# Optimization experiments

Hardware: AMD Instinct MI355X
Metric: run time of the kernel (lower is better)

## Reference

```python
import jax, jax.numpy as jnp
import numpy as np

N, E = 40000, 640000
IN, HID, OUT = 128, 128, 128


def _lin(key, fan_in, fan_out):
    bound = 1.0 / np.sqrt(fan_in)
    kw, kb = jax.random.split(key)
    W = jax.random.uniform(kw, (fan_in, fan_out), jnp.float32, -bound, bound)
    b = jax.random.uniform(kb, (fan_out,), jnp.float32, -bound, bound)
    return W, b


def setup_inputs() -> dict:
    key = jax.random.key(0)
    ks = jax.random.split(key, 10)
    node_feat = jax.random.normal(ks[0], (N, IN), jnp.float32)
    coord_feat = jax.random.normal(ks[1], (N, 3), jnp.float32)
    src = jax.random.randint(ks[2], (E,), 0, N, jnp.int32)
    dst = jax.random.randint(ks[3], (E,), 0, N, jnp.int32)
    # edge_mlp: Linear(2*IN+1 -> HID), SiLU, Linear(HID -> HID), SiLU
    We1, be1 = _lin(ks[4], 2 * IN + 1, HID)
    We2, be2 = _lin(ks[5], HID, HID)
    # node_mlp: Linear(IN+HID -> HID), SiLU, Linear(HID -> OUT)
    Wn1, bn1 = _lin(ks[6], IN + HID, HID)
    Wn2, bn2 = _lin(ks[7], HID, OUT)
    # coord_mlp: Linear(HID -> HID), SiLU, Linear(HID -> 1, bias=False)
    Wc1, bc1 = _lin(ks[8], HID, HID)
    Wc2, _ = _lin(ks[9], HID, 1)
    return {"node_feat": node_feat, "coord_feat": coord_feat, "src": src, "dst": dst,
            "We1": We1, "be1": be1, "We2": We2, "be2": be2,
            "Wn1": Wn1, "bn1": bn1, "Wn2": Wn2, "bn2": bn2,
            "Wc1": Wc1, "bc1": bc1, "Wc2": Wc2}


def reference(node_feat, coord_feat, src, dst,
              We1, be1, We2, be2, Wn1, bn1, Wn2, bn2, Wc1, bc1, Wc2):
    n = node_feat.shape[0]
    # edge gather: u_sub_v gives x_src - x_dst
    x_diff = coord_feat[src] - coord_feat[dst]                       # (E, 3)
    dist = jnp.sqrt(jnp.sum(x_diff * x_diff, axis=-1, keepdims=True))  # (E, 1)
    x_dir = x_diff / (dist + 1e-7)
    f = jnp.concatenate([node_feat[src], node_feat[dst], dist], axis=-1)  # (E, 2*IN+1)
    msg_h = jax.nn.silu(jax.nn.silu(f @ We1 + be1) @ We2 + be2)      # (E, HID)
    coef = jax.nn.silu(msg_h @ Wc1 + bc1) @ Wc2                      # (E, 1)
    msg_x = coef * x_dir                                             # (E, 3)
    # scatter-reduce to destination nodes: sum for h, mean for x
    h_neigh = jax.ops.segment_sum(msg_h, dst, num_segments=n)        # (N, HID)
    cnt = jax.ops.segment_sum(jnp.ones((dst.shape[0], 1), msg_x.dtype), dst, num_segments=n)
    x_neigh = jax.ops.segment_sum(msg_x, dst, num_segments=n) / jnp.maximum(cnt, 1.0)
    h = jax.nn.silu(jnp.concatenate([node_feat, h_neigh], axis=-1) @ Wn1 + bn1) @ Wn2 + bn2
    return h, coord_feat + x_neigh
```

## Files before the change

### kernel.cpp

```cpp
#include <hip/hip_runtime.h>
#include <hip/hip_bf16.h>
#include <math.h>
#include <stdint.h>

#define N_NODES 40000
#define N_EDGES 640000

typedef short short8 __attribute__((ext_vector_type(8)));
typedef float f32x4 __attribute__((ext_vector_type(4)));

__device__ __forceinline__ float silu(float x) {
    return __fdividef(x, 1.0f + __expf(-x));
}

__device__ __forceinline__ unsigned short f2bf(float f) {
    unsigned u = __float_as_uint(f);
    u += 0x7FFF + ((u >> 16) & 1);
    return (unsigned short)(u >> 16);
}
__device__ __forceinline__ float bf2f(unsigned short h) {
    return __uint_as_float(((unsigned)h) << 16);
}
__device__ __forceinline__ unsigned pk2bf(float a, float b) {
    __hip_bfloat162 h = __float22bfloat162_rn(make_float2(a, b));
    unsigned u;
    __builtin_memcpy(&u, &h, 4);
    return u;
}

__global__ __launch_bounds__(1024) void k_scan(const int* __restrict__ deg,
                                               int* __restrict__ row_start) {
    __shared__ int wsum[16];
    const int t = threadIdx.x;
    const int lane = t & 63, wid = t >> 6;
    int base = 0;
    if (t == 0) row_start[0] = 0;
    for (int off = 0; off < N_NODES; off += 1024) {
        int x = (off + t < N_NODES) ? deg[off + t] : 0;
#pragma unroll
        for (int s = 1; s < 64; s <<= 1) {
            const int u = __shfl_up(x, s, 64);
            if (lane >= s) x += u;
        }
        if (lane == 63) wsum[wid] = x;
        __syncthreads();
        if (wid == 0) {
            int ws = (lane < 16) ? wsum[lane] : 0;
#pragma unroll
            for (int s = 1; s < 16; s <<= 1) {
                const int u = __shfl_up(ws, s, 64);
                if (lane >= s) ws += u;
            }
            if (lane < 16) wsum[lane] = ws;
        }
        __syncthreads();
        const int wbase = (wid > 0) ? wsum[wid - 1] : 0;
        const int total = wsum[15];
        if (off + t < N_NODES) row_start[off + t + 1] = base + wbase + x;
        base += total;
        __syncthreads();
    }
}

__global__ __launch_bounds__(256) void k_fill(const int* __restrict__ dst,
                                              const int* __restrict__ row_start,
                                              int* __restrict__ cursor,
                                              int* __restrict__ elist) {
    const int e = blockIdx.x * 256 + threadIdx.x;
    if (e < N_EDGES) {
        const int d = dst[e];
        const int p = atomicAdd(&cursor[d], 1);
        elist[row_start[d] + p] = e;
    }
}

__global__ __launch_bounds__(128) void k_pack2(
    const float* __restrict__ We1, const float* __restrict__ We2,
    const float* __restrict__ Wc1, const float* __restrict__ Wn1,
    const float* __restrict__ Wn2,
    unsigned short* __restrict__ Wt_e1, unsigned short* __restrict__ Wt_e2,
    unsigned short* __restrict__ Wt_c1, unsigned short* __restrict__ Wt_n1,
    unsigned short* __restrict__ Wt_n2,
    int* __restrict__ deg, int* __restrict__ cursor, float* __restrict__ xs,
    float* __restrict__ hn) {
    const int b = blockIdx.x;
    const int t = threadIdx.x;
    Wt_e1[b * 128 + t] = f2bf(We1[(size_t)((b >> 7) * 128 + t) * 128 + (b & 127)]);
    if (b < 128) {
        Wt_e2[b * 128 + t] = f2bf(We2[(size_t)t * 128 + b]);
        Wt_c1[b * 128 + t] = f2bf(Wc1[(size_t)t * 128 + b]);
        Wt_n2[b * 128 + t] = f2bf(Wn2[(size_t)t * 128 + b]);
        Wt_n1[b * 256 + t] = f2bf(Wn1[(size_t)t * 128 + b]);
        Wt_n1[b * 256 + 128 + t] = f2bf(Wn1[(size_t)(128 + t) * 128 + b]);
    }
    const int gid = b * 128 + t;
    for (int i = gid; i < N_NODES; i += 32768) { deg[i] = 0; cursor[i] = 0; }
    for (int i = gid; i < N_NODES * 4; i += 32768) xs[i] = 0.0f;
    float4* hz = (float4*)hn;
    const float4 z4 = {0.f, 0.f, 0.f, 0.f};
    for (int i = gid; i < N_NODES * 32; i += 32768) hz[i] = z4;
}

__global__ __launch_bounds__(256) void k_cntpre(
    const float* __restrict__ nf, const unsigned short* __restrict__ Wt_e1,
    unsigned short* __restrict__ Pc,
    const int* __restrict__ dst, int* __restrict__ deg) {
    __shared__ __align__(16) unsigned short sNF[32][136];
    const int t = threadIdx.x;
    const int node0 = blockIdx.x * 32;
    {
        const int e0 = (blockIdx.x * 256 + t) * 2;
        const int d0 = dst[e0], d1 = dst[e0 + 1];
        atomicAdd(&deg[d0], 1);
        atomicAdd(&deg[d1], 1);
    }
    {
        const int m = t >> 3, kc = (t & 7) * 16;
        const float* sp = &nf[(size_t)(node0 + m) * 128 + kc];
        const float4 v0 = *(const float4*)(sp + 0);
        const float4 v1 = *(const float4*)(sp + 4);
        const float4 v2 = *(const float4*)(sp + 8);
        const float4 v3 = *(const float4*)(sp + 12);
        int4 o0, o1;
        o0.x = pk2bf(v0.x, v0.y); o0.y = pk2bf(v0.z, v0.w);
        o0.z = pk2bf(v1.x, v1.y); o0.w = pk2bf(v1.z, v1.w);
        o1.x = pk2bf(v2.x, v2.y); o1.y = pk2bf(v2.z, v2.w);
        o1.z = pk2bf(v3.x, v3.y); o1.w = pk2bf(v3.z, v3.w);
        *(int4*)&sNF[m][kc] = o0;
        *(int4*)&sNF[m][kc + 8] = o1;
    }
    __syncthreads();

    const int w = t >> 6, l = t & 63, c = l & 15, quad = l >> 4;
    const int n0 = w * 64;

    f32x4 acc[2][4];
#pragma unroll
    for (int mt = 0; mt < 2; mt++)
#pragma unroll
        for (int tile = 0; tile < 4; tile++) acc[mt][tile] = (f32x4){0.f, 0.f, 0.f, 0.f};

#pragma unroll
    for (int k0 = 0; k0 < 128; k0 += 32) {
        const short8 a0 = *(const short8*)&sNF[c][k0 + quad * 8];
        const short8 a1 = *(const short8*)&sNF[16 + c][k0 + quad * 8];
#pragma unroll
        for (int tile = 0; tile < 4; tile++) {
            const short8 b = *(const short8*)(Wt_e1 +
                ((size_t)(n0 + tile * 16 + c) << 7) + k0 + quad * 8);
            acc[0][tile] = __builtin_amdgcn_mfma_f32_16x16x32_bf16(a0, b, acc[0][tile], 0, 0, 0);
            acc[1][tile] = __builtin_amdgcn_mfma_f32_16x16x32_bf16(a1, b, acc[1][tile], 0, 0, 0);
        }
    }
#pragma unroll
    for (int mt = 0; mt < 2; mt++)
#pragma unroll
        for (int tile = 0; tile < 4; tile++) {
            const int col = n0 + tile * 16 + c;
            const unsigned p01 = pk2bf(acc[mt][tile][0], acc[mt][tile][1]);
            const unsigned p23 = pk2bf(acc[mt][tile][2], acc[mt][tile][3]);
            const int row = node0 + mt * 16 + quad * 4;
            Pc[(size_t)(row + 0) * 256 + col] = (unsigned short)p01;
            Pc[(size_t)(row + 1) * 256 + col] = (unsigned short)(p01 >> 16);
            Pc[(size_t)(row + 2) * 256 + col] = (unsigned short)p23;
            Pc[(size_t)(row + 3) * 256 + col] = (unsigned short)(p23 >> 16);
        }
}

__global__ __launch_bounds__(512) void k_edge5(
    const unsigned short* __restrict__ Pc, const float* __restrict__ coord,
    const int* __restrict__ src, const int* __restrict__ dst,
    const int* __restrict__ elist,
    const float* __restrict__ We1, const float* __restrict__ be1,
    const unsigned short* __restrict__ Wt_e2, const float* __restrict__ be2,
    const unsigned short* __restrict__ Wt_c1, const float* __restrict__ bc1,
    const float* __restrict__ Wc2,
    float* __restrict__ h_neigh, float* __restrict__ xs) {
    __shared__ __align__(16) unsigned short sT[128][136];
    __shared__ float scoefp[8][32];
    __shared__ float sw[128], sb[128];
    __shared__ float sdist[128];
    __shared__ float sxd[128][3];
    __shared__ int ssrc[128];
    __shared__ int sdst[128];

    const int t = threadIdx.x;
    const int e0 = blockIdx.x * 128;

    if (t < 128) {
        const int eid = elist[e0 + t];
        const int s = src[eid], d = dst[eid];
        ssrc[t] = s; sdst[t] = d;
        const float dx = coord[3 * s + 0] - coord[3 * d + 0];
        const float dy = coord[3 * s + 1] - coord[3 * d + 1];
        const float dz = coord[3 * s + 2] - coord[3 * d + 2];
        const float dist = sqrtf(dx * dx + dy * dy + dz * dz);
        sdist[t] = dist;
        const float inv = __fdividef(1.0f, dist + 1e-7f);
        sxd[t][0] = dx * inv; sxd[t][1] = dy * inv; sxd[t][2] = dz * inv;
    } else if (t < 160) {
        ((float4*)sw)[t - 128] = ((const float4*)(We1 + 256 * 128))[t - 128];
    } else if (t < 192) {
        ((float4*)sb)[t - 160] = ((const float4*)be1)[t - 160];
    }
    __syncthreads();

    {
        const int e = t >> 2;
        const int kc = (t & 3) * 32;
        const int s = ssrc[e], d = sdst[e];
        const float dist = sdist[e];
        const unsigned short* p1 = Pc + (size_t)s * 256 + kc;
        const unsigned short* p2 = Pc + (size_t)d * 256 + 128 + kc;
        short8 a[4], b[4];
#pragma unroll
        for (int i = 0; i < 4; i++) {
            a[i] = *(const short8*)(p1 + i * 8);
            b[i] = *(const short8*)(p2 + i * 8);
        }
#pragma unroll
        for (int i = 0; i < 4; i++) {
            float v[8];
#pragma unroll
            for (int kk = 0; kk < 8; kk++) {
                const int k = kc + i * 8 + kk;
                v[kk] = silu(bf2f((unsigned short)a[i][kk]) + bf2f((unsigned short)b[i][kk])
                             + dist * sw[k] + sb[k]);
            }
            int4 o;
            o.x = pk2bf(v[0], v[1]); o.y = pk2bf(v[2], v[3]);
            o.z = pk2bf(v[4], v[5]); o.w = pk2bf(v[6], v[7]);
            *(int4*)&sT[e][kc + i * 8] = o;
        }
    }
    __syncthreads();

    const int w = t >> 6;
    const int l = t & 63;
    const int h = w & 3;
    const int H = w >> 2;
    const int m0 = h * 32;
    const int n0 = H * 64;
    const int c = l & 15;
    const int quad = l >> 4;

    f32x4 acc1[2][4];
#pragma unroll
    for (int mt = 0; mt < 2; mt++)
#pragma unroll
        for (int tile = 0; tile < 4; tile++) acc1[mt][tile] = (f32x4){0.f, 0.f, 0.f, 0.f};
#pragma unroll
    for (int k0 = 0; k0 < 128; k0 += 32) {
        const short8 a0 = *(const short8*)&sT[m0 + c][k0 + quad * 8];
        const short8 a1 = *(const short8*)&sT[m0 + 16 + c][k0 + quad * 8];
#pragma unroll
        for (int tile = 0; tile < 4; tile++) {
            const short8 b = *(const short8*)(Wt_e2 +
                ((size_t)(n0 + tile * 16 + c) << 7) + k0 + quad * 8);
            acc1[0][tile] = __builtin_amdgcn_mfma_f32_16x16x32_bf16(a0, b, acc1[0][tile], 0, 0, 0);
            acc1[1][tile] = __builtin_amdgcn_mfma_f32_16x16x32_bf16(a1, b, acc1[1][tile], 0, 0, 0);
        }
    }
    __syncthreads();

#pragma unroll
    for (int mt = 0; mt < 2; mt++)
#pragma unroll
        for (int tile = 0; tile < 4; tile++) {
            const int col = n0 + tile * 16 + c;
            const float bb = be2[col];
            const unsigned p01 = pk2bf(silu(acc1[mt][tile][0] + bb), silu(acc1[mt][tile][1] + bb));
            const unsigned p23 = pk2bf(silu(acc1[mt][tile][2] + bb), silu(acc1[mt][tile][3] + bb));
            const int row = m0 + mt * 16 + quad * 4;
            sT[row + 0][col] = (unsigned short)p01;
            sT[row + 1][col] = (unsigned short)(p01 >> 16);
            sT[row + 2][col] = (unsigned short)p23;
            sT[row + 3][col] = (unsigned short)(p23 >> 16);
        }
    __syncthreads();

    {
        const int j = t & 127;
        const int q = t >> 7;
        const int eb = q * 32;
        float acc = bf2f(sT[eb][j]);
        int prev = sdst[eb];
        for (int e2 = eb + 1; e2 < eb + 32; e2++) {
            const int de = sdst[e2];
            if (de != prev) {
                atomicAdd(&h_neigh[(size_t)prev * 128 + j], acc);
                acc = 0.0f;
                prev = de;
            }
            acc += bf2f(sT[e2][j]);
        }
        atomicAdd(&h_neigh[(size_t)prev * 128 + j], acc);
    }

    {
        f32x4 acc[2][4];
#pragma unroll
        for (int mt = 0; mt < 2; mt++)
#pragma unroll
            for (int tile = 0; tile < 4; tile++) acc[mt][tile] = (f32x4){0.f, 0.f, 0.f, 0.f};
#pragma unroll
        for (int k0 = 0; k0 < 128; k0 += 32) {
            const short8 a0 = *(const short8*)&sT[m0 + c][k0 + quad * 8];
            const short8 a1 = *(const short8*)&sT[m0 + 16 + c][k0 + quad * 8];
#pragma unroll
            for (int tile = 0; tile < 4; tile++) {
                const short8 b = *(const short8*)(Wt_c1 +
                    ((size_t)(n0 + tile * 16 + c) << 7) + k0 + quad * 8);
                acc[0][tile] = __builtin_amdgcn_mfma_f32_16x16x32_bf16(a0, b, acc[0][tile], 0, 0, 0);
                acc[1][tile] = __builtin_amdgcn_mfma_f32_16x16x32_bf16(a1, b, acc[1][tile], 0, 0, 0);
            }
        }
        float part[2][4] = {{0.f, 0.f, 0.f, 0.f}, {0.f, 0.f, 0.f, 0.f}};
#pragma unroll
        for (int tile = 0; tile < 4; tile++) {
            const int col = n0 + tile * 16 + c;
            const float bc = bc1[col];
            const float wc = Wc2[col];
#pragma unroll
            for (int mt = 0; mt < 2; mt++)
#pragma unroll
                for (int r = 0; r < 4; r++)
                    part[mt][r] += silu(acc[mt][tile][r] + bc) * wc;
        }
#pragma unroll
        for (int off = 1; off < 16; off <<= 1) {
#pragma unroll
            for (int mt = 0; mt < 2; mt++)
#pragma unroll
                for (int r = 0; r < 4; r++)
                    part[mt][r] += __shfl_xor(part[mt][r], off, 64);
        }
        if (c == 0) {
#pragma unroll
            for (int mt = 0; mt < 2; mt++)
#pragma unroll
                for (int r = 0; r < 4; r++)
                    scoefp[w][mt * 16 + quad * 4 + r] = part[mt][r];
        }
    }

    if (l < 3) {
        const int cc = l;
        const int eb = h * 32;
        float acc = scoefp[w][0] * sxd[eb][cc];
        int prev = sdst[eb];
        for (int e2 = eb + 1; e2 < eb + 32; e2++) {
            const int de = sdst[e2];
            if (de != prev) {
                atomicAdd(&xs[(size_t)prev * 4 + cc], acc);
                acc = 0.0f;
                prev = de;
            }
            acc += scoefp[w][e2 & 31] * sxd[e2][cc];
        }
        atomicAdd(&xs[(size_t)prev * 4 + cc], acc);
    }
}

__global__ __launch_bounds__(256) void k_node(
    const float* __restrict__ nf, const float* __restrict__ coord,
    const float* __restrict__ hn, const float* __restrict__ xs,
    const int* __restrict__ row_start,
    const unsigned short* __restrict__ Wt_n1, const float* __restrict__ bn1,
    const unsigned short* __restrict__ Wt_n2, const float* __restrict__ bn2,
    float* __restrict__ out_h, float* __restrict__ out_x) {
    __shared__ __align__(16) unsigned short sAB[32][264];
    __shared__ __align__(16) unsigned short sH[32][136];
    const int t = threadIdx.x;
    const int node0 = blockIdx.x * 32;
    {
        const int m = t >> 3, kc = (t & 7) * 32;
        const float* base = (kc < 128) ? &nf[(size_t)(node0 + m) * 128 + kc]
                                       : &hn[(size_t)(node0 + m) * 128 + (kc - 128)];
#pragma unroll
        for (int kk = 0; kk < 32; kk += 8) {
            const float4 v0 = *(const float4*)(base + kk);
            const float4 v1 = *(const float4*)(base + kk + 4);
            int4 o;
            o.x = pk2bf(v0.x, v0.y); o.y = pk2bf(v0.z, v0.w);
            o.z = pk2bf(v1.x, v1.y); o.w = pk2bf(v1.z, v1.w);
            *(int4*)&sAB[m][kc + kk] = o;
        }
    }
    if (t < 96) {
        const int m = t / 3, cc = t - m * 3;
        const int i = node0 + m;
        const float cnt = (float)(row_start[i + 1] - row_start[i]);
        out_x[(size_t)i * 3 + cc] =
            coord[(size_t)i * 3 + cc] + __fdividef(xs[(size_t)i * 4 + cc], fmaxf(cnt, 1.0f));
    }
    __syncthreads();

    const int w = t >> 6, l = t & 63, c = l & 15, quad = l >> 4;
    const int n0 = w * 32;

    {
        f32x4 acc[2][2];
#pragma unroll
        for (int mt = 0; mt < 2; mt++)
#pragma unroll
            for (int tile = 0; tile < 2; tile++) acc[mt][tile] = (f32x4){0.f, 0.f, 0.f, 0.f};
#pragma unroll
        for (int k0 = 0; k0 < 256; k0 += 32) {
            const short8 a0 = *(const short8*)&sAB[c][k0 + quad * 8];
            const short8 a1 = *(const short8*)&sAB[16 + c][k0 + quad * 8];
#pragma unroll
            for (int tile = 0; tile < 2; tile++) {
                const short8 b = *(const short8*)(Wt_n1 +
                    ((size_t)(n0 + tile * 16 + c) << 8) + k0 + quad * 8);
                acc[0][tile] = __builtin_amdgcn_mfma_f32_16x16x32_bf16(a0, b, acc[0][tile], 0, 0, 0);
                acc[1][tile] = __builtin_amdgcn_mfma_f32_16x16x32_bf16(a1, b, acc[1][tile], 0, 0, 0);
            }
        }
#pragma unroll
        for (int mt = 0; mt < 2; mt++)
#pragma unroll
            for (int tile = 0; tile < 2; tile++) {
                const int col = n0 + tile * 16 + c;
                const float bb = bn1[col];
                const unsigned p01 = pk2bf(silu(acc[mt][tile][0] + bb), silu(acc[mt][tile][1] + bb));
                const unsigned p23 = pk2bf(silu(acc[mt][tile][2] + bb), silu(acc[mt][tile][3] + bb));
                const int row = mt * 16 + quad * 4;
                sH[row + 0][col] = (unsigned short)p01;
                sH[row + 1][col] = (unsigned short)(p01 >> 16);
                sH[row + 2][col] = (unsigned short)p23;
                sH[row + 3][col] = (unsigned short)(p23 >> 16);
            }
    }
    __syncthreads();

    {
        f32x4 acc[2][2];
#pragma unroll
        for (int mt = 0; mt < 2; mt++)
#pragma unroll
            for (int tile = 0; tile < 2; tile++) acc[mt][tile] = (f32x4){0.f, 0.f, 0.f, 0.f};
#pragma unroll
        for (int k0 = 0; k0 < 128; k0 += 32) {
            const short8 a0 = *(const short8*)&sH[c][k0 + quad * 8];
            const short8 a1 = *(const short8*)&sH[16 + c][k0 + quad * 8];
#pragma unroll
            for (int tile = 0; tile < 2; tile++) {
                const short8 b = *(const short8*)(Wt_n2 +
                    ((size_t)(n0 + tile * 16 + c) << 7) + k0 + quad * 8);
                acc[0][tile] = __builtin_amdgcn_mfma_f32_16x16x32_bf16(a0, b, acc[0][tile], 0, 0, 0);
                acc[1][tile] = __builtin_amdgcn_mfma_f32_16x16x32_bf16(a1, b, acc[1][tile], 0, 0, 0);
            }
        }
#pragma unroll
        for (int mt = 0; mt < 2; mt++)
#pragma unroll
            for (int tile = 0; tile < 2; tile++) {
                const int col = n0 + tile * 16 + c;
                const float bb = bn2[col];
#pragma unroll
                for (int r = 0; r < 4; r++) {
                    const int row = mt * 16 + quad * 4 + r;
                    out_h[(size_t)(node0 + row) * 128 + col] = acc[mt][tile][r] + bb;
                }
            }
    }
}

extern "C" void kernel_launch(void* const* d_in, const int* in_sizes, int n_in,
                              void* d_out, int out_size, void* d_ws, size_t ws_size,
                              hipStream_t stream) {
    const float* nf    = (const float*)d_in[0];
    const float* coord = (const float*)d_in[1];
    const int*   src   = (const int*)d_in[2];
    const int*   dst   = (const int*)d_in[3];
    const float* We1   = (const float*)d_in[4];
    const float* be1   = (const float*)d_in[5];
    const float* We2   = (const float*)d_in[6];
    const float* be2   = (const float*)d_in[7];
    const float* Wn1   = (const float*)d_in[8];
    const float* bn1   = (const float*)d_in[9];
    const float* Wn2   = (const float*)d_in[10];
    const float* bn2   = (const float*)d_in[11];
    const float* Wc1   = (const float*)d_in[12];
    const float* bc1   = (const float*)d_in[13];
    const float* Wc2   = (const float*)d_in[14];

    unsigned short* Pc = (unsigned short*)d_ws;
    float* hn = (float*)(Pc + (size_t)N_NODES * 256);
    float* xs = hn + (size_t)N_NODES * 128;
    int* deg       = (int*)(xs + (size_t)N_NODES * 4);
    int* row_start = deg + N_NODES;
    int* cursor    = row_start + N_NODES + 1;
    int* elist     = cursor + N_NODES;
    unsigned short* Wt_e1 = (unsigned short*)
        (((uintptr_t)(elist + N_EDGES) + 255) & ~(uintptr_t)255);
    unsigned short* Wt_e2 = Wt_e1 + 256 * 128;
    unsigned short* Wt_c1 = Wt_e2 + 128 * 128;
    unsigned short* Wt_n1 = Wt_c1 + 128 * 128;
    unsigned short* Wt_n2 = Wt_n1 + 128 * 256;

    float* out_h = (float*)d_out;
    float* out_x = out_h + (size_t)N_NODES * 128;

    k_pack2<<<256, 128, 0, stream>>>(We1, We2, Wc1, Wn1, Wn2,
                                     Wt_e1, Wt_e2, Wt_c1, Wt_n1, Wt_n2,
                                     deg, cursor, xs, hn);
    k_cntpre<<<N_NODES / 32, 256, 0, stream>>>(nf, Wt_e1, Pc, dst, deg);
    k_scan<<<1, 1024, 0, stream>>>(deg, row_start);
    k_fill<<<(N_EDGES + 255) / 256, 256, 0, stream>>>(dst, row_start, cursor, elist);
    k_edge5<<<N_EDGES / 128, 512, 0, stream>>>(Pc, coord, src, dst, elist,
                                               We1, be1, Wt_e2, be2, Wt_c1, bc1,
                                               Wc2, hn, xs);
    k_node<<<N_NODES / 32, 256, 0, stream>>>(nf, coord, hn, xs, row_start,
                                             Wt_n1, bn1, Wt_n2, bn2, out_h, out_x);
}
```

Baseline: 477.4 us.

## Store sorted src/dst pairs in fill, swizzle edge tiles, widen segmented reduction

k_fill now writes (src,dst) int2 pairs in dst-sorted order, so the edge kernel no longer does the indirect elist→src/dst gather. The serialized prologue phase where 128 threads computed coordinates is folded into the main gather: every thread loads its edge pair and computes distance itself. Block indices are remapped to spread tiles across XCDs, and the segmented h_neigh reduction now has each thread handle two columns over 16 edges using wave/lane variables. This adds redundant coordinate loads per edge (four threads each) and a larger sorted buffer, and relies on `w` and `l` being defined in the omitted code.

```diff
diff --git a/kernel.cpp b/kernel.cpp
--- a/kernel.cpp
+++ b/kernel.cpp
@@ -62,15 +62,16 @@
     }
 }
 
-__global__ __launch_bounds__(256) void k_fill(const int* __restrict__ dst,
+__global__ __launch_bounds__(256) void k_fill(const int* __restrict__ src,
+                                              const int* __restrict__ dst,
                                               const int* __restrict__ row_start,
                                               int* __restrict__ cursor,
-                                              int* __restrict__ elist) {
+                                              int2* __restrict__ sd) {
     const int e = blockIdx.x * 256 + threadIdx.x;
     if (e < N_EDGES) {
         const int d = dst[e];
         const int p = atomicAdd(&cursor[d], 1);
-        elist[row_start[d] + p] = e;
+        sd[row_start[d] + p] = make_int2(src[e], d);
     }
 }
 
@@ -167,10 +168,9 @@
         }
 }
 
-__global__ __launch_bounds__(512) void k_edge5(
+__global__ __launch_bounds__(512) void k_edge6(
     const unsigned short* __restrict__ Pc, const float* __restrict__ coord,
-    const int* __restrict__ src, const int* __restrict__ dst,
-    const int* __restrict__ elist,
+    const int2* __restrict__ sd,
     const float* __restrict__ We1, const float* __restrict__ be1,
     const unsigned short* __restrict__ Wt_e2, const float* __restrict__ be2,
     const unsigned short* __restrict__ Wt_c1, const float* __restrict__ bc1,
@@ -179,37 +179,34 @@
     __shared__ __align__(16) unsigned short sT[128][136];
     __shared__ float scoefp[8][32];
     __shared__ float sw[128], sb[128];
-    __shared__ float sdist[128];
     __shared__ float sxd[128][3];
-    __shared__ int ssrc[128];
     __shared__ int sdst[128];
 
     const int t = threadIdx.x;
-    const int e0 = blockIdx.x * 128;
-
-    if (t < 128) {
-        const int eid = elist[e0 + t];
-        const int s = src[eid], d = dst[eid];
-        ssrc[t] = s; sdst[t] = d;
-        const float dx = coord[3 * s + 0] - coord[3 * d + 0];
-        const float dy = coord[3 * s + 1] - coord[3 * d + 1];
-        const float dz = coord[3 * s + 2] - coord[3 * d + 2];
-        const float dist = sqrtf(dx * dx + dy * dy + dz * dz);
-        sdist[t] = dist;
-        const float inv = __fdividef(1.0f, dist + 1e-7f);
-        sxd[t][0] = dx * inv; sxd[t][1] = dy * inv; sxd[t][2] = dz * inv;
-    } else if (t < 160) {
-        ((float4*)sw)[t - 128] = ((const float4*)(We1 + 256 * 128))[t - 128];
-    } else if (t < 192) {
-        ((float4*)sb)[t - 160] = ((const float4*)be1)[t - 160];
+    const int tile_id = (blockIdx.x & 7) * 625 + (blockIdx.x >> 3);
+    const int e0 = tile_id * 128;
+
+    if (t < 32) {
+        ((float4*)sw)[t] = ((const float4*)(We1 + 256 * 128))[t];
+    } else if (t < 64) {
+        ((float4*)sb)[t - 32] = ((const float4*)be1)[t - 32];
     }
     __syncthreads();
 
     {
         const int e = t >> 2;
         const int kc = (t & 3) * 32;
-        const int s = ssrc[e], d = sdst[e];
-        const float dist = sdist[e];
+        const int2 p = sd[e0 + e];
+        const int s = p.x, d = p.y;
+        const float* cs = coord + 3 * (size_t)s;
+        const float* cd = coord + 3 * (size_t)d;
+        const float dx = cs[0] - cd[0], dy = cs[1] - cd[1], dz = cs[2] - cd[2];
+        const float dist = sqrtf(dx * dx + dy * dy + dz * dz);
+        if ((t & 3) == 0) {
+            sdst[e] = d;
+            const float inv = __fdividef(1.0f, dist + 1e-7f);
+            sxd[e][0] = dx * inv; sxd[e][1] = dy * inv; sxd[e][2] = dz * inv;
+        }
         const unsigned short* p1 = Pc + (size_t)s * 256 + kc;
         const unsigned short* p2 = Pc + (size_t)d * 256 + 128 + kc;
         short8 a[4], b[4];
@@ -280,21 +277,27 @@
     __syncthreads();
 
     {
-        const int j = t & 127;
-        const int q = t >> 7;
-        const int eb = q * 32;
-        float acc = bf2f(sT[eb][j]);
+        const int jp = (l) * 2;
+        const int q = w;
+        const int eb = q * 16;
+        const unsigned v0 = *(const unsigned*)&sT[eb][jp];
+        float acc0 = bf2f((unsigned short)v0);
+        float acc1 = bf2f((unsigned short)(v0 >> 16));
         int prev = sdst[eb];
-        for (int e2 = eb + 1; e2 < eb + 32; e2++) {
+        for (int e2 = eb + 1; e2 < eb + 16; e2++) {
             const int de = sdst[e2];
             if (de != prev) {
-                atomicAdd(&h_neigh[(size_t)prev * 128 + j], acc);
-                acc = 0.0f;
+                atomicAdd(&h_neigh[(size_t)prev * 128 + jp], acc0);
+                atomicAdd(&h_neigh[(size_t)prev * 128 + jp + 1], acc1);
+                acc0 = 0.0f; acc1 = 0.0f;
                 prev = de;
             }
-            acc += bf2f(sT[e2][j]);
-        }
-        atomicAdd(&h_neigh[(size_t)prev * 128 + j], acc);
+            const unsigned v = *(const unsigned*)&sT[e2][jp];
+            acc0 += bf2f((unsigned short)v);
+            acc1 += bf2f((unsigned short)(v >> 16));
+        }
+        atomicAdd(&h_neigh[(size_t)prev * 128 + jp], acc0);
+        atomicAdd(&h_neigh[(size_t)prev * 128 + jp + 1], acc1);
     }
 
     {
@@ -492,9 +495,9 @@
     int* deg       = (int*)(xs + (size_t)N_NODES * 4);
     int* row_start = deg + N_NODES;
     int* cursor    = row_start + N_NODES + 1;
-    int* elist     = cursor + N_NODES;
+    int2* sd       = (int2*)(((uintptr_t)(cursor + N_NODES) + 15) & ~(uintptr_t)15);
     unsigned short* Wt_e1 = (unsigned short*)
-        (((uintptr_t)(elist + N_EDGES) + 255) & ~(uintptr_t)255);
+        (((uintptr_t)(sd + N_EDGES) + 255) & ~(uintptr_t)255);
     unsigned short* Wt_e2 = Wt_e1 + 256 * 128;
     unsigned short* Wt_c1 = Wt_e2 + 128 * 128;
     unsigned short* Wt_n1 = Wt_c1 + 128 * 128;
@@ -508,8 +511,8 @@
                                      deg, cursor, xs, hn);
     k_cntpre<<<N_NODES / 32, 256, 0, stream>>>(nf, Wt_e1, Pc, dst, deg);
     k_scan<<<1, 1024, 0, stream>>>(deg, row_start);
-    k_fill<<<(N_EDGES + 255) / 256, 256, 0, stream>>>(dst, row_start, cursor, elist);
-    k_edge5<<<N_EDGES / 128, 512, 0, stream>>>(Pc, coord, src, dst, elist,
+    k_fill<<<(N_EDGES + 255) / 256, 256, 0, stream>>>(src, dst, row_start, cursor, sd);
+    k_edge6<<<N_EDGES / 128, 512, 0, stream>>>(Pc, coord, sd,
                                                We1, be1, Wt_e2, be2, Wt_c1, bc1,
                                                Wc2, hn, xs);
     k_node<<<N_NODES / 32, 256, 0, stream>>>(nf, coord, hn, xs, row_start,
```

Result: no change. 486.3 us (+1.9%).
